# Kernel tuning notes

Measured on AMD Instinct MI355X. Metric: run time of the kernel, lower is better.

The kernel has to match this reference:

```python
import jax, jax.numpy as jnp
import numpy as np

B, T, V, E, H = 128, 512, 32000, 256, 128


def _lstm(xw, U, b, reverse):
    """Run an LSTM over time.
    xw: [T, B, 4H] precomputed input projections; U: [H, 4H]; b: [4H].
    Returns (hs [T,B,H], h_T [B,H], c_T [B,H]). Keras gate order i,f,g,o.
    """
    Hd = U.shape[0]
    Bd = xw.shape[1]

    def step(carry, xw_t):
        h, c = carry
        z = xw_t + h @ U + b  # [B, 4H]
        i, f, g, o = jnp.split(z, 4, axis=-1)
        i = jax.nn.sigmoid(i)
        f = jax.nn.sigmoid(f)
        g = jnp.tanh(g)
        o = jax.nn.sigmoid(o)
        c = f * c + i * g
        h = o * jnp.tanh(c)
        return (h, c), h

    h0 = jnp.zeros((Bd, Hd), xw.dtype)
    (hT, cT), hs = jax.lax.scan(step, (h0, h0), xw, reverse=reverse)
    return hs, hT, cT


def setup_inputs() -> dict:
    key = jax.random.key(0)
    ks = jax.random.split(key, 8)
    tokens = jax.random.randint(ks[0], (B, T), 0, V, dtype=jnp.int64)
    emb = jax.random.uniform(ks[1], (V, E), jnp.float32, -0.05, 0.05)
    s_in = 1.0 / np.sqrt(E)
    s_rec = 1.0 / np.sqrt(H)
    W_fw = jax.random.normal(ks[2], (E, 4 * H), jnp.float32) * s_in
    U_fw = jax.random.normal(ks[3], (H, 4 * H), jnp.float32) * s_rec
    b_fw = jnp.zeros((4 * H,), jnp.float32).at[H:2 * H].set(1.0)  # unit forget bias
    W_bw = jax.random.normal(ks[4], (E, 4 * H), jnp.float32) * s_in
    U_bw = jax.random.normal(ks[5], (H, 4 * H), jnp.float32) * s_rec
    b_bw = jnp.zeros((4 * H,), jnp.float32).at[H:2 * H].set(1.0)
    return {"tokens": tokens, "emb": emb,
            "W_fw": W_fw, "U_fw": U_fw, "b_fw": b_fw,
            "W_bw": W_bw, "U_bw": U_bw, "b_bw": b_bw}


def reference(tokens, emb, W_fw, U_fw, b_fw, W_bw, U_bw, b_bw):
    # Embedding lookup (dropout layers are identity at inference)
    x = emb[tokens]                    # [B, T, E]
    xt = jnp.swapaxes(x, 0, 1)         # [T, B, E] time-major for scan
    # Precompute input projections as one big GEMM per direction
    hs_fw, h_fw, c_fw = _lstm(xt @ W_fw, U_fw, b_fw, reverse=False)
    hs_bw, h_bw, c_bw = _lstm(xt @ W_bw, U_bw, b_bw, reverse=True)
    out = jnp.concatenate([hs_fw, hs_bw], axis=-1)  # [T, B, 2H]
    out = jnp.swapaxes(out, 0, 1)                    # [B, T, 2H]
    return out, (h_fw, c_fw), (h_bw, c_bw)
```

## Files before the change

### kernel.cpp

```cpp
#include <hip/hip_runtime.h>
#include <hip/hip_bf16.h>


typedef short short8 __attribute__((ext_vector_type(8)));
typedef float f32x4 __attribute__((ext_vector_type(4)));

#define GLL16(g, l)                                                        \
  __builtin_amdgcn_global_load_lds(                                        \
      (const __attribute__((address_space(1))) void*)(g),                  \
      (__attribute__((address_space(3))) void*)(l), 16, 0, 0)

__device__ __forceinline__ unsigned short f2bf(float f) {
  __hip_bfloat16 h = __float2bfloat16(f);
  return __builtin_bit_cast(unsigned short, h);
}

__global__ void prep_emb(const float4* __restrict__ in,
                         ushort4* __restrict__ outp, int n4) {
  int i = blockIdx.x * blockDim.x + threadIdx.x;
  if (i < n4) {
    float4 v = in[i];
    ushort4 o;
    o.x = f2bf(v.x); o.y = f2bf(v.y); o.z = f2bf(v.z); o.w = f2bf(v.w);
    outp[i] = o;
  }
}

__global__ void prep_wt(const float* __restrict__ Wfw,
                        const float* __restrict__ Wbw,
                        __hip_bfloat16* __restrict__ Wt) {
  int n = blockIdx.x;
  int k = threadIdx.x;
  const float* W = (n < 512) ? Wfw : Wbw;
  Wt[n * 256 + k] = __float2bfloat16(W[k * 512 + (n & 511)]);
}

__global__ __launch_bounds__(256) void gemm_xw(
    const int* __restrict__ tokens, const __hip_bfloat16* __restrict__ embb,
    const __hip_bfloat16* __restrict__ Wt, __hip_bfloat16* __restrict__ xw) {
  __shared__ __attribute__((aligned(16))) __hip_bfloat16 As[128 * 32];
  __shared__ __attribute__((aligned(16))) __hip_bfloat16 Bs[128 * 32];
  const int tid = threadIdx.x;
  const int bm = blockIdx.x;
  const int bn = blockIdx.y;
  const int lane = tid & 63, w = tid >> 6;

  const int ar = tid >> 2;
  const int kcol = (tid & 3) * 8;
  const long r0 = (long)bm * 128 + ar;
  const int tok0 = tokens[r0];
  const int tok1 = tokens[r0 + 64];
  const __hip_bfloat16* a0 = embb + (size_t)tok0 * 256 + kcol;
  const __hip_bfloat16* a1 = embb + (size_t)tok1 * 256 + kcol;
  const __hip_bfloat16* bs0 = Wt + ((size_t)bn * 128 + ar) * 256 + kcol;
  const __hip_bfloat16* bs1 = bs0 + 64 * 256;
  __hip_bfloat16* As_d0 = As + tid * 8;
  __hip_bfloat16* As_d1 = As + 2048 + tid * 8;
  __hip_bfloat16* Bs_d0 = Bs + tid * 8;
  __hip_bfloat16* Bs_d1 = Bs + 2048 + tid * 8;

  f32x4 acc[4][4];
#pragma unroll
  for (int i = 0; i < 4; ++i)
#pragma unroll
    for (int j = 0; j < 4; ++j) acc[i][j] = (f32x4){0.f, 0.f, 0.f, 0.f};

  const int fm = (w >> 1) * 64, fn = (w & 1) * 64;
  const int lr = lane & 15, lk = (lane >> 4) * 8;

  for (int kk = 0; kk < 8; ++kk) {
    GLL16(a0 + kk * 32, As_d0);
    GLL16(a1 + kk * 32, As_d1);
    GLL16(bs0 + kk * 32, Bs_d0);
    GLL16(bs1 + kk * 32, Bs_d1);
    __syncthreads();
    short8 af[4], bfr[4];
#pragma unroll
    for (int i = 0; i < 4; ++i)
      af[i] = *(const short8*)(As + (fm + 16 * i + lr) * 32 + lk);
#pragma unroll
    for (int j = 0; j < 4; ++j)
      bfr[j] = *(const short8*)(Bs + (fn + 16 * j + lr) * 32 + lk);
#pragma unroll
    for (int i = 0; i < 4; ++i)
#pragma unroll
      for (int j = 0; j < 4; ++j)
        acc[i][j] = __builtin_amdgcn_mfma_f32_16x16x32_bf16(af[i], bfr[j],
                                                            acc[i][j], 0, 0, 0);
    __syncthreads();
  }

  const int orow = (lane >> 4) * 4;
#pragma unroll
  for (int i = 0; i < 4; ++i)
#pragma unroll
    for (int j = 0; j < 4; ++j)
#pragma unroll
      for (int r = 0; r < 4; ++r) {
        int row_local = fm + 16 * i + orow + r;
        int col_local = fn + 16 * j + (lane & 15);
        size_t rg = (size_t)bm * 128 + row_local;
        int ng = bn * 128 + col_local;
        size_t addr = (size_t)(ng >> 9) * 33554432ull + rg * 512 + (ng & 511);
        xw[addr] = __float2bfloat16(acc[i][j][r]);
      }
}

__global__ __launch_bounds__(512, 2) void lstm_rec(
    const float* __restrict__ U_fw, const float* __restrict__ b_fw,
    const float* __restrict__ U_bw, const float* __restrict__ b_bw,
    const __hip_bfloat16* __restrict__ xw, float* __restrict__ out) {
  __shared__ __attribute__((aligned(16))) float h_lds[128];
  __shared__ float g_lds[512];
  const int tid = threadIdx.x;
  const int dir = blockIdx.x >> 7;
  const int b = blockIdx.x & 127;
  const float* U = dir ? U_bw : U_fw;
  const float bias = (dir ? b_bw : b_fw)[tid];

  float Uc[128];
#pragma unroll
  for (int k = 0; k < 128; ++k) Uc[k] = U[k * 512 + tid];

  if (tid < 128) h_lds[tid] = 0.f;
  float c = 0.f, hfin = 0.f;
  __syncthreads();

  const __hip_bfloat16* xb =
      xw + (size_t)dir * 33554432ull + (size_t)b * 262144ull + tid;
  float* outb = out + (size_t)b * 512 * 256 + dir * 128;

  int t = dir ? 511 : 0;
  const int st = dir ? -1 : 1;
  __hip_bfloat16 xc = xb[(size_t)t * 512];
  const float4* h4 = (const float4*)h_lds;
  const int grp = tid >> 7;

  for (int it = 0; it < 512; ++it) {
    const int tn = (it == 511) ? t : (t + st);
    __hip_bfloat16 xn = xb[(size_t)tn * 512];
    float a0 = 0.f, a1 = 0.f, a2 = 0.f, a3 = 0.f;
#pragma unroll
    for (int k4 = 0; k4 < 32; ++k4) {
      float4 hv = h4[k4];
      a0 = fmaf(hv.x, Uc[4 * k4 + 0], a0);
      a1 = fmaf(hv.y, Uc[4 * k4 + 1], a1);
      a2 = fmaf(hv.z, Uc[4 * k4 + 2], a2);
      a3 = fmaf(hv.w, Uc[4 * k4 + 3], a3);
    }
    float z = __bfloat162float(xc) + bias + ((a0 + a1) + (a2 + a3));
    float act = (grp == 2) ? tanhf(z) : 1.f / (1.f + expf(-z));
    g_lds[tid] = act;
    __syncthreads();
    if (tid < 128) {
      c = g_lds[128 + tid] * c + g_lds[tid] * g_lds[256 + tid];
      float h = g_lds[384 + tid] * tanhf(c);
      hfin = h;
      h_lds[tid] = h;
      outb[(size_t)t * 256 + tid] = h;
    }
    __syncthreads();
    xc = xn;
    t = tn;
  }
  if (tid < 128) {
    float* o2 = out + 16777216;
    o2[dir * 32768 + b * 128 + tid] = hfin;
    o2[dir * 32768 + 16384 + b * 128 + tid] = c;
  }
}

extern "C" void kernel_launch(void* const* d_in, const int* in_sizes, int n_in,
                              void* d_out, int out_size, void* d_ws,
                              size_t ws_size, hipStream_t stream) {
  const int* tokens = (const int*)d_in[0];
  const float* emb = (const float*)d_in[1];
  const float* W_fw = (const float*)d_in[2];
  const float* U_fw = (const float*)d_in[3];
  const float* b_fw = (const float*)d_in[4];
  const float* W_bw = (const float*)d_in[5];
  const float* U_bw = (const float*)d_in[6];
  const float* b_bw = (const float*)d_in[7];
  float* out = (float*)d_out;

  char* ws = (char*)d_ws;
  __hip_bfloat16* embb = (__hip_bfloat16*)(ws);
  __hip_bfloat16* Wt = (__hip_bfloat16*)(ws + 16384000);
  __hip_bfloat16* xw = (__hip_bfloat16*)(ws + 16908288);

  prep_emb<<<8000, 256, 0, stream>>>((const float4*)emb, (ushort4*)embb,
                                     2048000);
  prep_wt<<<1024, 256, 0, stream>>>(W_fw, W_bw, Wt);
  gemm_xw<<<dim3(512, 8), 256, 0, stream>>>(tokens, embb, Wt, xw);
  lstm_rec<<<256, 512, 0, stream>>>(U_fw, b_fw, U_bw, b_bw, xw, out);
}
```

Before: 644.7 us.

## Pre-transpose recurrent weights, use fast activations, and move output store past barrier

Adds a prep kernel that rearranges U into a k4-interleaved layout so each thread loads its 128 recurrent weights with vector loads, and relaxes launch bounds to one block per SIMD group to give more registers. It replaces tanhf and expf with __expf-based approximations in the serial recurrence and moves the global h store after the second barrier so it overlaps with the next step. The scratch for U reuses the workspace region of the bf16 embedding copy, which is no longer needed once the GEMM has run. The fast activations cost some accuracy, and fewer blocks per CU reduces latency hiding.

```diff
diff --git a/kernel.cpp b/kernel.cpp
--- a/kernel.cpp
+++ b/kernel.cpp
@@ -13,6 +13,13 @@
 __device__ __forceinline__ unsigned short f2bf(float f) {
   __hip_bfloat16 h = __float2bfloat16(f);
   return __builtin_bit_cast(unsigned short, h);
+}
+
+__device__ __forceinline__ float fast_sigmoid(float z) {
+  return 1.f / (1.f + __expf(-z));
+}
+__device__ __forceinline__ float fast_tanh(float z) {
+  return 1.f - 2.f / (__expf(2.f * z) + 1.f);
 }
 
 __global__ void prep_emb(const float4* __restrict__ in,
@@ -106,24 +113,37 @@
       }
 }
 
-__global__ __launch_bounds__(512, 2) void lstm_rec(
-    const float* __restrict__ U_fw, const float* __restrict__ b_fw,
-    const float* __restrict__ U_bw, const float* __restrict__ b_bw,
-    const __hip_bfloat16* __restrict__ xw, float* __restrict__ out) {
+__global__ void prep_ut(const float* __restrict__ Ufw,
+                        const float* __restrict__ Ubw,
+                        float* __restrict__ Ut) {
+  int idx = blockIdx.x * 512 + threadIdx.x;
+  int j = idx & 3;
+  int dc = (idx >> 2) & 1023;
+  int k4 = idx >> 12;
+  int k = 4 * k4 + j;
+  int c = dc & 511;
+  const float* U = (dc >> 9) ? Ubw : Ufw;
+  Ut[idx] = U[k * 512 + c];
+}
+
+__global__ __launch_bounds__(512, 1) void lstm_rec(
+    const float* __restrict__ Ut, const float* __restrict__ b_fw,
+    const float* __restrict__ b_bw, const __hip_bfloat16* __restrict__ xw,
+    float* __restrict__ out) {
   __shared__ __attribute__((aligned(16))) float h_lds[128];
   __shared__ float g_lds[512];
   const int tid = threadIdx.x;
   const int dir = blockIdx.x >> 7;
   const int b = blockIdx.x & 127;
-  const float* U = dir ? U_bw : U_fw;
   const float bias = (dir ? b_bw : b_fw)[tid];
 
-  float Uc[128];
-#pragma unroll
-  for (int k = 0; k < 128; ++k) Uc[k] = U[k * 512 + tid];
+  f32x4 Uc4[32];
+#pragma unroll
+  for (int k4 = 0; k4 < 32; ++k4)
+    Uc4[k4] = *(const f32x4*)(Ut + ((size_t)k4 * 1024 + dir * 512 + tid) * 4);
 
   if (tid < 128) h_lds[tid] = 0.f;
-  float c = 0.f, hfin = 0.f;
+  float c = 0.f, h = 0.f, hfin = 0.f;
   __syncthreads();
 
   const __hip_bfloat16* xb =
@@ -143,23 +163,24 @@
 #pragma unroll
     for (int k4 = 0; k4 < 32; ++k4) {
       float4 hv = h4[k4];
-      a0 = fmaf(hv.x, Uc[4 * k4 + 0], a0);
-      a1 = fmaf(hv.y, Uc[4 * k4 + 1], a1);
-      a2 = fmaf(hv.z, Uc[4 * k4 + 2], a2);
-      a3 = fmaf(hv.w, Uc[4 * k4 + 3], a3);
+      f32x4 u = Uc4[k4];
+      a0 = fmaf(hv.x, u.x, a0);
+      a1 = fmaf(hv.y, u.y, a1);
+      a2 = fmaf(hv.z, u.z, a2);
+      a3 = fmaf(hv.w, u.w, a3);
     }
     float z = __bfloat162float(xc) + bias + ((a0 + a1) + (a2 + a3));
-    float act = (grp == 2) ? tanhf(z) : 1.f / (1.f + expf(-z));
+    float act = (grp == 2) ? fast_tanh(z) : fast_sigmoid(z);
     g_lds[tid] = act;
     __syncthreads();
     if (tid < 128) {
       c = g_lds[128 + tid] * c + g_lds[tid] * g_lds[256 + tid];
-      float h = g_lds[384 + tid] * tanhf(c);
+      h = g_lds[384 + tid] * fast_tanh(c);
       hfin = h;
       h_lds[tid] = h;
-      outb[(size_t)t * 256 + tid] = h;
     }
     __syncthreads();
+    if (tid < 128) outb[(size_t)t * 256 + tid] = h;
     xc = xn;
     t = tn;
   }
@@ -187,10 +208,12 @@
   __hip_bfloat16* embb = (__hip_bfloat16*)(ws);
   __hip_bfloat16* Wt = (__hip_bfloat16*)(ws + 16384000);
   __hip_bfloat16* xw = (__hip_bfloat16*)(ws + 16908288);
+  float* Ut = (float*)(ws);
 
   prep_emb<<<8000, 256, 0, stream>>>((const float4*)emb, (ushort4*)embb,
                                      2048000);
   prep_wt<<<1024, 256, 0, stream>>>(W_fw, W_bw, Wt);
   gemm_xw<<<dim3(512, 8), 256, 0, stream>>>(tokens, embb, Wt, xw);
-  lstm_rec<<<256, 512, 0, stream>>>(U_fw, b_fw, U_bw, b_bw, xw, out);
-}
+  prep_ut<<<256, 512, 0, stream>>>(U_fw, U_bw, Ut);
+  lstm_rec<<<256, 512, 0, stream>>>(Ut, b_fw, b_bw, xw, out);
+}
```

Measured after the change: 641.5 us. Within noise of the previous version (-0.5%).
